# Optimization experiments

Hardware: AMD Instinct MI355X
Metric: run time of the kernel (lower is better)

## Reference

```python
import jax, jax.numpy as jnp
import numpy as np

IGNORE_INDEX = -100


def setup_inputs() -> dict:
    key = jax.random.key(0)
    k1, k2, k3 = jax.random.split(key, 3)
    BT, H, V = 2048, 2048, 128000
    x = jax.random.normal(k1, (BT, H), dtype=jnp.float32)
    weight = jax.random.normal(k2, (V, H), dtype=jnp.float32) * (1.0 / np.sqrt(H))
    target = jax.random.randint(k3, (BT,), 0, V, dtype=jnp.int64)
    return {"x": x, "weight": weight, "target": target}


def reference(x, weight, target):
    # Fused linear + cross-entropy forward (reduction='mean').
    # logits: [BT, V], accumulated in fp32 like the helion kernel.
    logits = jnp.einsum("bh,vh->bv", x.astype(jnp.float32), weight.astype(jnp.float32))
    lse = jax.nn.logsumexp(logits, axis=-1)  # [BT]
    target_logit = jnp.take_along_axis(logits, target[:, None], axis=-1)[:, 0]
    valid = (target != IGNORE_INDEX)
    nll = (lse - target_logit) * valid.astype(jnp.float32)  # [BT]
    n_non_ignore = valid.sum().astype(jnp.float32)
    loss = nll.sum() / n_non_ignore
    return loss.astype(x.dtype), lse
```

## Files before the change

### kernel.cpp

```cpp
#include <hip/hip_runtime.h>
#include <hip/hip_bf16.h>


typedef __bf16 bf16x8 __attribute__((ext_vector_type(8)));
typedef float f32x16 __attribute__((ext_vector_type(16)));

#define BM 128
#define BN 128
#define BK 32
#define LDK 40

__device__ __forceinline__ unsigned pkbf(float a, float b) {
  __hip_bfloat162 h = __float22bfloat162_rn(float2{a, b});
  unsigned r;
  __builtin_memcpy(&r, &h, 4);
  return r;
}

__device__ __forceinline__ void gl16(const void* g, const void* l) {
  using GP = const unsigned __attribute__((address_space(1)))*;
  using LP = unsigned __attribute__((address_space(3)))*;
  __builtin_amdgcn_global_load_lds((GP)(unsigned long long)g,
                                   (LP)(unsigned)(unsigned long long)l, 16, 0, 0);
}

__global__ __launch_bounds__(256)
void k_cvt256(const float* __restrict__ src, __bf16* __restrict__ dst, int H, int NT)
{
  const int bid = blockIdx.x;
  const int kt = bid % NT;
  const int r = threadIdx.x;
  const float* s = src + (size_t)((bid / NT) * 256 + r) * H + kt * 64;
  __bf16* d = dst + (size_t)bid * 16384;
  #pragma unroll
  for (int j = 0; j < 8; ++j) {
    float4 f0 = ((const float4*)s)[2 * j];
    float4 f1 = ((const float4*)s)[2 * j + 1];
    uint4 p;
    p.x = pkbf(f0.x, f0.y); p.y = pkbf(f0.z, f0.w);
    p.z = pkbf(f1.x, f1.y); p.w = pkbf(f1.z, f1.w);
    *(uint4*)(d + (j >> 2) * 8192 + (j & 3) * 2048 + r * 8) = p;
  }
}

__global__ __launch_bounds__(256)
void k_tgt(const float* __restrict__ x, const float* __restrict__ w,
           const int* __restrict__ tgt, float* __restrict__ ws_t, int H)
{
  const int row  = blockIdx.x * 4 + (threadIdx.x >> 6);
  const int lane = threadIdx.x & 63;
  const int tv = tgt[row];
  if (tv == -100) { if (lane == 0) ws_t[row] = 0.f; return; }
  const float* xr = x + (size_t)row * H;
  const float* wr = w + (size_t)tv * H;
  float acc = 0.f;
  for (int j = lane * 4; j < H; j += 256) {
    float4 a = *(const float4*)(xr + j);
    float4 b = *(const float4*)(wr + j);
    acc += a.x * b.x + a.y * b.y + a.z * b.z + a.w * b.w;
  }
  #pragma unroll
  for (int m = 1; m < 64; m <<= 1) acc += __shfl_xor(acc, m, 64);
  if (lane == 0) ws_t[row] = acc;
}

#define VM4 asm volatile("s_waitcnt vmcnt(4)" ::: "memory");
#define VM0 asm volatile("s_waitcnt vmcnt(0)" ::: "memory");
#define NOVM

#define PHASE(KB, VMW)                                                          \
  {                                                                             \
    _Pragma("unroll")                                                           \
    for (int i = 0; i < 4; ++i)                                                 \
      _Pragma("unroll")                                                         \
      for (int ks = 0; ks < 2; ++ks)                                            \
        aF[i][ks] = *(const bf16x8*)&A[(KB) * 8192 + (ks * 2 + hi) * 2048 +     \
                                       (wr * 128 + i * 32 + rlo) * 8];          \
    _Pragma("unroll")                                                           \
    for (int nf = 0; nf < 2; ++nf)                                              \
      _Pragma("unroll")                                                         \
      for (int ks = 0; ks < 2; ++ks)                                            \
        bF[nf][ks] = *(const bf16x8*)&B[(KB) * 8192 + (ks * 2 + hi) * 2048 +    \
                                        (wc * 64 + nf * 32 + rlo) * 8];         \
    if (do_stage) {                                                             \
      stage_half(nbuf, kt + 1, (KB) * 2);                                       \
      stage_half(nbuf, kt + 1, (KB) * 2 + 1);                                   \
    }                                                                           \
    __builtin_amdgcn_s_barrier();                                               \
    __builtin_amdgcn_s_setprio(1);                                              \
    _Pragma("unroll")                                                           \
    for (int i = 0; i < 4; ++i)                                                 \
      _Pragma("unroll")                                                         \
      for (int nf = 0; nf < 2; ++nf)                                            \
        _Pragma("unroll")                                                       \
        for (int ks = 0; ks < 2; ++ks)                                          \
          acc[i][nf] = __builtin_amdgcn_mfma_f32_32x32x16_bf16(                 \
              aF[i][ks], bF[nf][ks], acc[i][nf], 0, 0, 0);                      \
    __builtin_amdgcn_s_setprio(0);                                              \
    VMW                                                                         \
    __builtin_amdgcn_s_barrier();                                               \
  }

__global__ __launch_bounds__(512, 2)
void k_gemm8(const __bf16* __restrict__ xb, const __bf16* __restrict__ wb,
             float* __restrict__ ws_m, float* __restrict__ ws_s,
             int NT, int NCB, int ROWB)
{
  __shared__ __bf16 As[2][16384];
  __shared__ __bf16 Bs[2][16384];

  int wg = blockIdx.x;
  const int nwg = gridDim.x;
  if ((nwg & 7) == 0) wg = (wg & 7) * (nwg >> 3) + (wg >> 3);
  const int rowb = wg % ROWB;
  const int cb   = wg / ROWB;
  const int row0 = rowb * 256;

  const int t    = threadIdx.x;
  const int lane = t & 63;
  const int wv   = t >> 6;
  const int wr   = wv >> 2;
  const int wc   = wv & 3;
  const int rlo  = lane & 31;
  const int hi   = lane >> 5;

  const __bf16* ga = xb + (size_t)(rowb * NT) * 16384;
  const __bf16* gb = wb + (size_t)(cb * NT) * 16384;

  auto stage_half = [&](int buf, int kt2, int h) {
    const int kh = h >> 1;
    const __bf16* gsrc = ((h & 1) ? gb : ga) + (size_t)kt2 * 16384 + kh * 8192;
    __bf16* lbase = ((h & 1) ? &Bs[buf][0] : &As[buf][0]) + kh * 8192;
    #pragma unroll
    for (int c = 0; c < 2; ++c)
      gl16(gsrc + c * 4096 + wv * 512 + lane * 8,
           lbase + c * 4096 + wv * 512);
  };

  #pragma unroll
  for (int h = 0; h < 4; ++h) stage_half(0, 0, h);
  VM4
  __builtin_amdgcn_s_barrier();

  f32x16 acc[4][2] = {};
  bf16x8 aF[4][2], bF[2][2];

  int cur = 0, kt = 0;
  const __bf16* A;
  const __bf16* B;
  bool do_stage = true;
  int nbuf;

  for (kt = 0; kt < NT - 1; ++kt) {
    A = &As[cur][0]; B = &Bs[cur][0]; nbuf = cur ^ 1;
    PHASE(0, VM4)
    PHASE(1, VM4)
    cur ^= 1;
  }
  A = &As[cur][0]; B = &Bs[cur][0]; nbuf = cur ^ 1; do_stage = false;
  PHASE(0, VM0)
  PHASE(1, NOVM)

  __syncthreads();

  float* redM = (float*)&As[0][0];
  float* redS = redM + 1024;
  #pragma unroll
  for (int mr = 0; mr < 4; ++mr) {
    #pragma unroll
    for (int reg = 0; reg < 16; ++reg) {
      const int rl = wr * 128 + mr * 32 + (reg & 3) + 8 * (reg >> 2) + 4 * hi;
      const float v0 = acc[mr][0][reg], v1 = acc[mr][1][reg];
      float mx = fmaxf(v0, v1);
      #pragma unroll
      for (int m = 1; m < 32; m <<= 1) mx = fmaxf(mx, __shfl_xor(mx, m, 64));
      float sv = expf(v0 - mx) + expf(v1 - mx);
      #pragma unroll
      for (int m = 1; m < 32; m <<= 1) sv += __shfl_xor(sv, m, 64);
      if (rlo == 0) { redM[wc * 256 + rl] = mx; redS[wc * 256 + rl] = sv; }
    }
  }
  __syncthreads();
  if (t < 256) {
    const float m0 = redM[t], m1 = redM[256 + t], m2 = redM[512 + t], m3 = redM[768 + t];
    float M = fmaxf(fmaxf(m0, m1), fmaxf(m2, m3));
    float S = redS[t] * expf(m0 - M) + redS[256 + t] * expf(m1 - M)
            + redS[512 + t] * expf(m2 - M) + redS[768 + t] * expf(m3 - M);
    const int grow = row0 + t;
    ws_m[(size_t)grow * NCB + cb] = M;
    ws_s[(size_t)grow * NCB + cb] = S;
  }
}

__global__ __launch_bounds__(256, 2)
void k_gemm_lse(const float* __restrict__ x, const float* __restrict__ w,
                const int* __restrict__ tgt,
                float* __restrict__ ws_m, float* __restrict__ ws_s,
                float* __restrict__ ws_t,
                int H, int NCB, int ROWB)
{
  __shared__ unsigned short As[2][BM * LDK];
  __shared__ unsigned short Bs[2][BN * LDK];

  const int bid  = blockIdx.x;
  const int rowb = bid % ROWB;
  const int cb   = bid / ROWB;
  const int row0 = rowb * BM;
  const int col0 = cb * BN;

  const int t    = threadIdx.x;
  const int lane = t & 63;
  const int wv   = t >> 6;
  const int sr = t >> 1;
  const int sk = (t & 1) * 16;

  const float* xa = x + (size_t)(row0 + sr) * H + sk;
  const float* wb = w + (size_t)(col0 + sr) * H + sk;

  float4 ra[4], rb[4];
  #pragma unroll
  for (int i = 0; i < 4; ++i) {
    ra[i] = *(const float4*)(xa + i * 4);
    rb[i] = *(const float4*)(wb + i * 4);
  }

  auto stage = [&](int buf) {
    uint4 p0, p1;
    p0.x = pkbf(ra[0].x, ra[0].y); p0.y = pkbf(ra[0].z, ra[0].w);
    p0.z = pkbf(ra[1].x, ra[1].y); p0.w = pkbf(ra[1].z, ra[1].w);
    p1.x = pkbf(ra[2].x, ra[2].y); p1.y = pkbf(ra[2].z, ra[2].w);
    p1.z = pkbf(ra[3].x, ra[3].y); p1.w = pkbf(ra[3].z, ra[3].w);
    *(uint4*)&As[buf][sr * LDK + sk]     = p0;
    *(uint4*)&As[buf][sr * LDK + sk + 8] = p1;
    p0.x = pkbf(rb[0].x, rb[0].y); p0.y = pkbf(rb[0].z, rb[0].w);
    p0.z = pkbf(rb[1].x, rb[1].y); p0.w = pkbf(rb[1].z, rb[1].w);
    p1.x = pkbf(rb[2].x, rb[2].y); p1.y = pkbf(rb[2].z, rb[2].w);
    p1.z = pkbf(rb[3].x, rb[3].y); p1.w = pkbf(rb[3].z, rb[3].w);
    *(uint4*)&Bs[buf][sr * LDK + sk]     = p0;
    *(uint4*)&Bs[buf][sr * LDK + sk + 8] = p1;
  };

  stage(0);
  __syncthreads();

  f32x16 acc[4] = {};
  const int rlo = lane & 31;
  const int hi  = lane >> 5;
  const int NT  = H / BK;
  int cur = 0;

  for (int kt = 0; kt < NT; ++kt) {
    const bool pf = (kt + 1 < NT);
    if (pf) {
      xa += BK; wb += BK;
      #pragma unroll
      for (int i = 0; i < 4; ++i) {
        ra[i] = *(const float4*)(xa + i * 4);
        rb[i] = *(const float4*)(wb + i * 4);
      }
    }
    const unsigned short* A = As[cur];
    const unsigned short* B = Bs[cur];
    #pragma unroll
    for (int ks = 0; ks < 2; ++ks) {
      const int koff = ks * 16 + hi * 8;
      bf16x8 a = *(const bf16x8*)&A[(wv * 32 + rlo) * LDK + koff];
      #pragma unroll
      for (int nf = 0; nf < 4; ++nf) {
        bf16x8 b = *(const bf16x8*)&B[(nf * 32 + rlo) * LDK + koff];
        acc[nf] = __builtin_amdgcn_mfma_f32_32x32x16_bf16(a, b, acc[nf], 0, 0, 0);
      }
    }
    if (pf) stage(cur ^ 1);
    __syncthreads();
    cur ^= 1;
  }

  #pragma unroll
  for (int reg = 0; reg < 16; ++reg) {
    const int row = wv * 32 + (reg & 3) + 8 * (reg >> 2) + 4 * hi;
    float mx = fmaxf(fmaxf(acc[0][reg], acc[1][reg]), fmaxf(acc[2][reg], acc[3][reg]));
    #pragma unroll
    for (int m = 1; m < 32; m <<= 1) mx = fmaxf(mx, __shfl_xor(mx, m, 64));
    float s = 0.f;
    #pragma unroll
    for (int nf = 0; nf < 4; ++nf) s += expf(acc[nf][reg] - mx);
    #pragma unroll
    for (int m = 1; m < 32; m <<= 1) s += __shfl_xor(s, m, 64);
    const int grow = row0 + row;
    if (rlo == 0) {
      ws_m[(size_t)grow * NCB + cb] = mx;
      ws_s[(size_t)grow * NCB + cb] = s;
    }
    const int tv = tgt[grow];
    #pragma unroll
    for (int nf = 0; nf < 4; ++nf) {
      if (tv == col0 + nf * 32 + rlo) ws_t[grow] = acc[nf][reg];
    }
  }
}

__global__ void k_rowlse(const float* __restrict__ ws_m, const float* __restrict__ ws_s,
                         const float* __restrict__ ws_t, const int* __restrict__ tgt,
                         float* __restrict__ out, float* __restrict__ ws_nll, int NCB)
{
  const int row = blockIdx.x;
  const int t = threadIdx.x;
  const float* pm = ws_m + (size_t)row * NCB;
  const float* ps = ws_s + (size_t)row * NCB;
  __shared__ float red[8];

  float M = -3.0e38f;
  for (int j = t; j < NCB; j += 256) M = fmaxf(M, pm[j]);
  #pragma unroll
  for (int m = 1; m < 64; m <<= 1) M = fmaxf(M, __shfl_xor(M, m, 64));
  if ((t & 63) == 0) red[t >> 6] = M;
  __syncthreads();
  M = fmaxf(fmaxf(red[0], red[1]), fmaxf(red[2], red[3]));

  float S = 0.f;
  for (int j = t; j < NCB; j += 256) S += ps[j] * expf(pm[j] - M);
  #pragma unroll
  for (int m = 1; m < 64; m <<= 1) S += __shfl_xor(S, m, 64);
  if ((t & 63) == 0) red[4 + (t >> 6)] = S;
  __syncthreads();

  if (t == 0) {
    S = red[4] + red[5] + red[6] + red[7];
    const float lse = M + logf(S);
    out[1 + row] = lse;
    const int tv = tgt[row];
    ws_nll[row] = (tv != -100) ? (lse - ws_t[row]) : 0.f;
  }
}

__global__ void k_loss(const float* __restrict__ ws_nll, const int* __restrict__ tgt,
                       float* __restrict__ out, int BT)
{
  const int t = threadIdx.x;
  float s = 0.f, c = 0.f;
  for (int i = t; i < BT; i += 256) {
    s += ws_nll[i];
    c += (tgt[i] != -100) ? 1.f : 0.f;
  }
  __shared__ float rs[4], rc[4];
  #pragma unroll
  for (int m = 1; m < 64; m <<= 1) { s += __shfl_xor(s, m, 64); c += __shfl_xor(c, m, 64); }
  if ((t & 63) == 0) { rs[t >> 6] = s; rc[t >> 6] = c; }
  __syncthreads();
  if (t == 0) {
    s = rs[0] + rs[1] + rs[2] + rs[3];
    c = rc[0] + rc[1] + rc[2] + rc[3];
    out[0] = s / c;
  }
}

extern "C" void kernel_launch(void* const* d_in, const int* in_sizes, int n_in,
                              void* d_out, int out_size, void* d_ws, size_t ws_size,
                              hipStream_t stream)
{
  const float* x  = (const float*)d_in[0];
  const float* w  = (const float*)d_in[1];
  const int* tgt  = (const int*)d_in[2];
  float* out      = (float*)d_out;

  const int BT = in_sizes[2];
  const int H  = in_sizes[0] / BT;
  const int V  = in_sizes[1] / H;

  const int NT    = H / 64;
  const int ROWB  = BT / 256;
  const int NCB   = V / 256;

  const size_t bf_elems   = (size_t)BT * H + (size_t)V * H;
  const size_t need_bytes = bf_elems * 2 + ((size_t)2 * BT * NCB + 2 * (size_t)BT) * 4;

  if (ws_size >= need_bytes && (BT % 256) == 0 && (V % 256) == 0 && (H % 64) == 0) {
    __bf16* x_bf = (__bf16*)d_ws;
    __bf16* w_bf = x_bf + (size_t)BT * H;
    float* ws_m   = (float*)(w_bf + (size_t)V * H);
    float* ws_s   = ws_m + (size_t)BT * NCB;
    float* ws_t   = ws_s + (size_t)BT * NCB;
    float* ws_nll = ws_t + BT;

    k_cvt256<<<(V / 256) * NT, 256, 0, stream>>>(w, w_bf, H, NT);
    k_cvt256<<<(BT / 256) * NT, 256, 0, stream>>>(x, x_bf, H, NT);
    k_tgt<<<BT / 4, 256, 0, stream>>>(x, w, tgt, ws_t, H);
    k_gemm8<<<ROWB * NCB, 512, 0, stream>>>(x_bf, w_bf, ws_m, ws_s, NT, NCB, ROWB);
    k_rowlse<<<BT, 256, 0, stream>>>(ws_m, ws_s, ws_t, tgt, out, ws_nll, NCB);
    k_loss<<<1, 256, 0, stream>>>(ws_nll, tgt, out, BT);
  } else {
    const int ROWB1 = BT / BM;
    const int NCB1  = V / BN;
    float* ws_m   = (float*)d_ws;
    float* ws_s   = ws_m + (size_t)BT * NCB1;
    float* ws_t   = ws_s + (size_t)BT * NCB1;
    float* ws_nll = ws_t + BT;

    k_gemm_lse<<<ROWB1 * NCB1, 256, 0, stream>>>(x, w, tgt, ws_m, ws_s, ws_t, H, NCB1, ROWB1);
    k_rowlse<<<BT, 256, 0, stream>>>(ws_m, ws_s, ws_t, tgt, out, ws_nll, NCB1);
    k_loss<<<1, 256, 0, stream>>>(ws_nll, tgt, out, BT);
  }
}
```

Measured before the change: 1.624 ms.

## Switch GEMM to 16x16x32 MFMA with four-slot LDS pipeline

Replaces the 32x32x16 MFMA tiling with 16x16x32 MFMAs over an 8x4 accumulator grid per wave. The double-buffered 64-wide K stages become a four-slot ring of 32-wide K slices, prefetched three slots ahead, with wait counts adjusted. The aim is deeper global-to-LDS prefetch so memory latency is hidden behind MFMA work. The cost is more barriers per K step, an extra A-fragment reload per slot, and a new H%128 requirement for the fast path.

```diff
diff --git a/kernel.cpp b/kernel.cpp
--- a/kernel.cpp
+++ b/kernel.cpp
@@ -3,6 +3,7 @@
 
 
 typedef __bf16 bf16x8 __attribute__((ext_vector_type(8)));
+typedef float f32x4  __attribute__((ext_vector_type(4)));
 typedef float f32x16 __attribute__((ext_vector_type(16)));
 
 #define BM 128
@@ -64,50 +65,57 @@
   if (lane == 0) ws_t[row] = acc;
 }
 
+#define VM8 asm volatile("s_waitcnt vmcnt(8)" ::: "memory");
 #define VM4 asm volatile("s_waitcnt vmcnt(4)" ::: "memory");
 #define VM0 asm volatile("s_waitcnt vmcnt(0)" ::: "memory");
 #define NOVM
 
-#define PHASE(KB, VMW)                                                          \
+#define SLOT(SL, DO_ST, ST_S, WAITM)                                            \
   {                                                                             \
+    const __bf16* Ab = &As[SL][0];                                              \
+    const __bf16* Bb = &Bs[SL][0];                                              \
     _Pragma("unroll")                                                           \
-    for (int i = 0; i < 4; ++i)                                                 \
-      _Pragma("unroll")                                                         \
-      for (int ks = 0; ks < 2; ++ks)                                            \
-        aF[i][ks] = *(const bf16x8*)&A[(KB) * 8192 + (ks * 2 + hi) * 2048 +     \
-                                       (wr * 128 + i * 32 + rlo) * 8];          \
+    for (int m = 0; m < 4; ++m)                                                 \
+      aF[m] = *(const bf16x8*)&Ab[kcoff + (arow + m * 16) * 8];                 \
     _Pragma("unroll")                                                           \
-    for (int nf = 0; nf < 2; ++nf)                                              \
-      _Pragma("unroll")                                                         \
-      for (int ks = 0; ks < 2; ++ks)                                            \
-        bF[nf][ks] = *(const bf16x8*)&B[(KB) * 8192 + (ks * 2 + hi) * 2048 +    \
-                                        (wc * 64 + nf * 32 + rlo) * 8];         \
-    if (do_stage) {                                                             \
-      stage_half(nbuf, kt + 1, (KB) * 2);                                       \
-      stage_half(nbuf, kt + 1, (KB) * 2 + 1);                                   \
-    }                                                                           \
+    for (int n = 0; n < 4; ++n)                                                 \
+      bF[n] = *(const bf16x8*)&Bb[kcoff + (bcol + n * 16) * 8];                 \
+    if (DO_ST) stage_slot(ST_S);                                                \
     __builtin_amdgcn_s_barrier();                                               \
+    asm volatile("s_waitcnt lgkmcnt(0)" ::: "memory");                          \
     __builtin_amdgcn_s_setprio(1);                                              \
     _Pragma("unroll")                                                           \
-    for (int i = 0; i < 4; ++i)                                                 \
+    for (int m = 0; m < 4; ++m)                                                 \
       _Pragma("unroll")                                                         \
-      for (int nf = 0; nf < 2; ++nf)                                            \
-        _Pragma("unroll")                                                       \
-        for (int ks = 0; ks < 2; ++ks)                                          \
-          acc[i][nf] = __builtin_amdgcn_mfma_f32_32x32x16_bf16(                 \
-              aF[i][ks], bF[nf][ks], acc[i][nf], 0, 0, 0);                      \
+      for (int n = 0; n < 4; ++n)                                               \
+        acc[m][n] = __builtin_amdgcn_mfma_f32_16x16x32_bf16(aF[m], bF[n],       \
+                                                            acc[m][n], 0, 0, 0);\
     __builtin_amdgcn_s_setprio(0);                                              \
-    VMW                                                                         \
     __builtin_amdgcn_s_barrier();                                               \
+    _Pragma("unroll")                                                           \
+    for (int m = 0; m < 4; ++m)                                                 \
+      aF[m] = *(const bf16x8*)&Ab[kcoff + (arow + (m + 4) * 16) * 8];           \
+    __builtin_amdgcn_s_barrier();                                               \
+    asm volatile("s_waitcnt lgkmcnt(0)" ::: "memory");                          \
+    __builtin_amdgcn_s_setprio(1);                                              \
+    _Pragma("unroll")                                                           \
+    for (int m = 0; m < 4; ++m)                                                 \
+      _Pragma("unroll")                                                         \
+      for (int n = 0; n < 4; ++n)                                               \
+        acc[m + 4][n] = __builtin_amdgcn_mfma_f32_16x16x32_bf16(aF[m], bF[n],   \
+                                                         acc[m + 4][n], 0, 0, 0);\
+    __builtin_amdgcn_s_setprio(0);                                              \
+    WAITM                                                                       \
+    __builtin_amdgcn_s_barrier();                                               \
   }
 
 __global__ __launch_bounds__(512, 2)
-void k_gemm8(const __bf16* __restrict__ xb, const __bf16* __restrict__ wb,
-             float* __restrict__ ws_m, float* __restrict__ ws_s,
-             int NT, int NCB, int ROWB)
-{
-  __shared__ __bf16 As[2][16384];
-  __shared__ __bf16 Bs[2][16384];
+void k_gemm16(const __bf16* __restrict__ xb, const __bf16* __restrict__ wb,
+              float* __restrict__ ws_m, float* __restrict__ ws_s,
+              int NT, int NCB, int ROWB)
+{
+  __shared__ __bf16 As[4][8192];
+  __shared__ __bf16 Bs[4][8192];
 
   int wg = blockIdx.x;
   const int nwg = gridDim.x;
@@ -121,74 +129,78 @@
   const int wv   = t >> 6;
   const int wr   = wv >> 2;
   const int wc   = wv & 3;
-  const int rlo  = lane & 31;
-  const int hi   = lane >> 5;
+
+  const int kcoff = (lane >> 4) * 2048;
+  const int arow  = wr * 128 + (lane & 15);
+  const int bcol  = wc * 64 + (lane & 15);
 
   const __bf16* ga = xb + (size_t)(rowb * NT) * 16384;
   const __bf16* gb = wb + (size_t)(cb * NT) * 16384;
 
-  auto stage_half = [&](int buf, int kt2, int h) {
-    const int kh = h >> 1;
-    const __bf16* gsrc = ((h & 1) ? gb : ga) + (size_t)kt2 * 16384 + kh * 8192;
-    __bf16* lbase = ((h & 1) ? &Bs[buf][0] : &As[buf][0]) + kh * 8192;
-    #pragma unroll
-    for (int c = 0; c < 2; ++c)
-      gl16(gsrc + c * 4096 + wv * 512 + lane * 8,
-           lbase + c * 4096 + wv * 512);
+  auto stage_slot = [&](int s) {
+    const int ph = s & 3;
+    const size_t off = (size_t)(s >> 1) * 16384 + (size_t)(s & 1) * 8192
+                     + wv * 512 + lane * 8;
+    const __bf16* a = ga + off;
+    const __bf16* b = gb + off;
+    gl16(a,        &As[ph][wv * 512]);
+    gl16(a + 4096, &As[ph][4096 + wv * 512]);
+    gl16(b,        &Bs[ph][wv * 512]);
+    gl16(b + 4096, &Bs[ph][4096 + wv * 512]);
   };
 
-  #pragma unroll
-  for (int h = 0; h < 4; ++h) stage_half(0, 0, h);
-  VM4
+  const int S = NT * 2;
+
+  stage_slot(0); stage_slot(1); stage_slot(2);
+  VM8
   __builtin_amdgcn_s_barrier();
 
-  f32x16 acc[4][2] = {};
-  bf16x8 aF[4][2], bF[2][2];
-
-  int cur = 0, kt = 0;
-  const __bf16* A;
-  const __bf16* B;
-  bool do_stage = true;
-  int nbuf;
-
-  for (kt = 0; kt < NT - 1; ++kt) {
-    A = &As[cur][0]; B = &Bs[cur][0]; nbuf = cur ^ 1;
-    PHASE(0, VM4)
-    PHASE(1, VM4)
-    cur ^= 1;
-  }
-  A = &As[cur][0]; B = &Bs[cur][0]; nbuf = cur ^ 1; do_stage = false;
-  PHASE(0, VM0)
-  PHASE(1, NOVM)
+  f32x4 acc[8][4] = {};
+  bf16x8 aF[4], bF[4];
+
+  for (int g = 0; g < (S - 4) / 4; ++g) {
+    const int j0 = g * 4;
+    SLOT(0, true, j0 + 3, VM8)
+    SLOT(1, true, j0 + 4, VM8)
+    SLOT(2, true, j0 + 5, VM8)
+    SLOT(3, true, j0 + 6, VM8)
+  }
+  SLOT(0, true,  S - 1, VM8)
+  SLOT(1, false, 0,     VM4)
+  SLOT(2, false, 0,     VM0)
+  SLOT(3, false, 0,     NOVM)
 
   __syncthreads();
 
   float* redM = (float*)&As[0][0];
   float* redS = redM + 1024;
-  #pragma unroll
-  for (int mr = 0; mr < 4; ++mr) {
-    #pragma unroll
-    for (int reg = 0; reg < 16; ++reg) {
-      const int rl = wr * 128 + mr * 32 + (reg & 3) + 8 * (reg >> 2) + 4 * hi;
-      const float v0 = acc[mr][0][reg], v1 = acc[mr][1][reg];
-      float mx = fmaxf(v0, v1);
+  const int g4 = (lane >> 4) * 4;
+  #pragma unroll
+  for (int m = 0; m < 8; ++m) {
+    #pragma unroll
+    for (int r = 0; r < 4; ++r) {
+      const int rl = wr * 128 + m * 16 + g4 + r;
+      float mx = fmaxf(fmaxf(acc[m][0][r], acc[m][1][r]),
+                       fmaxf(acc[m][2][r], acc[m][3][r]));
       #pragma unroll
-      for (int m = 1; m < 32; m <<= 1) mx = fmaxf(mx, __shfl_xor(mx, m, 64));
-      float sv = expf(v0 - mx) + expf(v1 - mx);
+      for (int sh = 1; sh < 16; sh <<= 1) mx = fmaxf(mx, __shfl_xor(mx, sh, 64));
+      float sv = 0.f;
       #pragma unroll
-      for (int m = 1; m < 32; m <<= 1) sv += __shfl_xor(sv, m, 64);
-      if (rlo == 0) { redM[wc * 256 + rl] = mx; redS[wc * 256 + rl] = sv; }
+      for (int n = 0; n < 4; ++n) sv += expf(acc[m][n][r] - mx);
+      #pragma unroll
+      for (int sh = 1; sh < 16; sh <<= 1) sv += __shfl_xor(sv, sh, 64);
+      if ((lane & 15) == 0) { redM[wc * 256 + rl] = mx; redS[wc * 256 + rl] = sv; }
     }
   }
   __syncthreads();
   if (t < 256) {
     const float m0 = redM[t], m1 = redM[256 + t], m2 = redM[512 + t], m3 = redM[768 + t];
     float M = fmaxf(fmaxf(m0, m1), fmaxf(m2, m3));
-    float S = redS[t] * expf(m0 - M) + redS[256 + t] * expf(m1 - M)
-            + redS[512 + t] * expf(m2 - M) + redS[768 + t] * expf(m3 - M);
+    float S2 = redS[t] * expf(m0 - M) + redS[256 + t] * expf(m1 - M)
+             + redS[512 + t] * expf(m2 - M) + redS[768 + t] * expf(m3 - M);
     const int grow = row0 + t;
     ws_m[(size_t)grow * NCB + cb] = M;
-    ws_s[(size_t)grow * NCB + cb] = S;
+    ws_s[(size_t)grow * NCB + cb] = S2;
   }
 }
 
@@ -375,7 +387,7 @@
   const size_t bf_elems   = (size_t)BT * H + (size_t)V * H;
   const size_t need_bytes = bf_elems * 2 + ((size_t)2 * BT * NCB + 2 * (size_t)BT) * 4;
 
-  if (ws_size >= need_bytes && (BT % 256) == 0 && (V % 256) == 0 && (H % 64) == 0) {
+  if (ws_size >= need_bytes && (BT % 256) == 0 && (V % 256) == 0 && (H % 128) == 0) {
     __bf16* x_bf = (__bf16*)d_ws;
     __bf16* w_bf = x_bf + (size_t)BT * H;
     float* ws_m   = (float*)(w_bf + (size_t)V * H);
@@ -386,7 +398,7 @@
     k_cvt256<<<(V / 256) * NT, 256, 0, stream>>>(w, w_bf, H, NT);
     k_cvt256<<<(BT / 256) * NT, 256, 0, stream>>>(x, x_bf, H, NT);
     k_tgt<<<BT / 4, 256, 0, stream>>>(x, w, tgt, ws_t, H);
-    k_gemm8<<<ROWB * NCB, 512, 0, stream>>>(x_bf, w_bf, ws_m, ws_s, NT, NCB, ROWB);
+    k_gemm16<<<ROWB * NCB, 512, 0, stream>>>(x_bf, w_bf, ws_m, ws_s, NT, NCB, ROWB);
     k_rowlse<<<BT, 256, 0, stream>>>(ws_m, ws_s, ws_t, tgt, out, ws_nll, NCB);
     k_loss<<<1, 256, 0, stream>>>(ws_nll, tgt, out, BT);
   } else {
```

Measured after the change: 1.377 ms. 1.18x faster.
